# Kernel optimization log

Hardware: AMD Instinct MI355X
Metric: run time of the kernel (lower is better)

## Reference

```python
import jax, jax.numpy as jnp
import numpy as np

B, S, D = 8, 4096, 1024
EPS = 1e-8  # torch F.cosine_similarity default eps


def setup_inputs() -> dict:
    key = jax.random.key(0)
    kx, kwq, kbq, kwk, kbk = jax.random.split(key, 5)
    bound = 1.0 / np.sqrt(D)  # torch nn.Linear default init
    return {
        "x": jax.random.normal(kx, (B, S, D), dtype=jnp.float32),
        "Wq": jax.random.uniform(kwq, (D, D), jnp.float32, -bound, bound),
        "bq": jax.random.uniform(kbq, (D,), jnp.float32, -bound, bound),
        "Wk": jax.random.uniform(kwk, (D, D), jnp.float32, -bound, bound),
        "bk": jax.random.uniform(kbk, (D,), jnp.float32, -bound, bound),
    }


def reference(x, Wq, bq, Wk, bk):
    # ---- RoutingModule ----
    q = jnp.einsum("bsd,ed->bse", x, Wq) + bq                      # [B,S,D]
    x_roll = jnp.roll(x, shift=1, axis=1)                           # roll along seq
    k = jnp.einsum("bsd,ed->bse", x_roll, Wk) + bk                  # [B,S,D]
    qn = q / jnp.maximum(jnp.linalg.norm(q, axis=-1, keepdims=True), EPS)
    kn = k / jnp.maximum(jnp.linalg.norm(k, axis=-1, keepdims=True), EPS)
    cosine_sim = jnp.sum(qn * kn, axis=-1)                          # [B,S]
    p = 0.5 * (1.0 - cosine_sim)
    p = p.at[:, 0].set(1.0)
    b = (p >= 0.5).astype(x.dtype)                                  # [B,S]

    # ---- ragged compaction into padded buffer ----
    # Stable argsort moves selected positions to the front, preserving order.
    order = jnp.argsort(1.0 - b, axis=1)                            # [B,S] int
    gathered = jnp.take_along_axis(x, order[:, :, None], axis=1)    # [B,S,D]
    counts = jnp.sum(b, axis=1).astype(jnp.int32)                   # [B]
    valid = jnp.arange(S)[None, :] < counts[:, None]                # [B,S]
    # Padded to S (static max possible length) for jit-compatibility; torch
    # trims to the batch max, but all rows beyond each count are zeros here too.
    selected_padded = jnp.where(valid[:, :, None], gathered, 0.0)   # [B,S,D]
    return selected_padded, p, b
```

## Files before the change

### kernel.cpp

```cpp
#include <hip/hip_runtime.h>
#include <stdint.h>

#define Bb 8
#define Ss 4096
#define Dd 1024
#define Mm (Bb*Ss)
#define Nn (2*Dd)
#define Kk Dd

typedef _Float16 half8 __attribute__((ext_vector_type(8)));
typedef _Float16 half4v __attribute__((ext_vector_type(4)));
typedef float f32x4 __attribute__((ext_vector_type(4)));

#define LO_SCALE 2048.0f
#define INV_LO_SCALE (1.0f/2048.0f)

__device__ __forceinline__ void gld_lds16(const void* g, void* l) {
  __builtin_amdgcn_global_load_lds(
      (const __attribute__((address_space(1))) unsigned int*)g,
      (__attribute__((address_space(3))) unsigned int*)l, 16, 0, 0);
}

__global__ void split_kernel(const float* __restrict__ src,
                             _Float16* __restrict__ hi,
                             _Float16* __restrict__ lo, int n4) {
  int i = blockIdx.x * 256 + threadIdx.x;
  if (i >= n4) return;
  float4 v = ((const float4*)src)[i];
  _Float16 h0 = (_Float16)v.x, h1 = (_Float16)v.y, h2 = (_Float16)v.z, h3 = (_Float16)v.w;
  _Float16 l0 = (_Float16)((v.x - (float)h0) * LO_SCALE);
  _Float16 l1 = (_Float16)((v.y - (float)h1) * LO_SCALE);
  _Float16 l2 = (_Float16)((v.z - (float)h2) * LO_SCALE);
  _Float16 l3 = (_Float16)((v.w - (float)h3) * LO_SCALE);
  ((half4v*)hi)[i] = (half4v){h0, h1, h2, h3};
  ((half4v*)lo)[i] = (half4v){l0, l1, l2, l3};
}

__global__ __launch_bounds__(256, 2)
void gemm_split(const _Float16* __restrict__ AhG, const _Float16* __restrict__ AlG,
                const _Float16* __restrict__ BhG, const _Float16* __restrict__ BlG,
                const float* __restrict__ bq, const float* __restrict__ bk,
                float* __restrict__ C) {
  __shared__ __align__(16) _Float16 AsH[128 * 32];
  __shared__ __align__(16) _Float16 AsL[128 * 32];
  __shared__ __align__(16) _Float16 BsH[128 * 32];
  __shared__ __align__(16) _Float16 BsL[128 * 32];

  const int tid  = threadIdx.x;
  const int wave = tid >> 6;
  const int lane = tid & 63;
  const int m0 = blockIdx.y * 128;
  const int n0 = blockIdx.x * 128;
  const int wm = (wave >> 1) * 64;
  const int wn = (wave & 1) * 64;

  f32x4 accH[4][4];
  f32x4 accX[4][4];
#pragma unroll
  for (int i = 0; i < 4; ++i)
#pragma unroll
    for (int j = 0; j < 4; ++j) {
      accH[i][j] = (f32x4){0.f, 0.f, 0.f, 0.f};
      accX[i][j] = (f32x4){0.f, 0.f, 0.f, 0.f};
    }

  const int srow = (lane >> 2);
  const int scol = (lane & 3) * 8;

  for (int kt = 0; kt < Kk / 32; ++kt) {
    const int k0 = kt * 32;
#pragma unroll
    for (int it = 0; it < 2; ++it) {
      const int r = wave * 32 + it * 16 + srow;
      const int ldsbase = (wave * 32 + it * 16) * 32;
      const size_t ga = (size_t)(m0 + r) * Kk + k0 + scol;
      const size_t gb = (size_t)(n0 + r) * Kk + k0 + scol;
      gld_lds16(AhG + ga, &AsH[ldsbase]);
      gld_lds16(AlG + ga, &AsL[ldsbase]);
      gld_lds16(BhG + gb, &BsH[ldsbase]);
      gld_lds16(BlG + gb, &BsL[ldsbase]);
    }
    __syncthreads();

    const int fr = (lane & 15);
    const int fk = (lane >> 4) * 8;
    half8 bh[4], bl[4];
#pragma unroll
    for (int j = 0; j < 4; ++j) {
      bh[j] = *(const half8*)&BsH[(wn + 16 * j + fr) * 32 + fk];
      bl[j] = *(const half8*)&BsL[(wn + 16 * j + fr) * 32 + fk];
    }
#pragma unroll
    for (int i = 0; i < 4; ++i) {
      half8 ah = *(const half8*)&AsH[(wm + 16 * i + fr) * 32 + fk];
      half8 al = *(const half8*)&AsL[(wm + 16 * i + fr) * 32 + fk];
#pragma unroll
      for (int j = 0; j < 4; ++j) {
        accH[i][j] = __builtin_amdgcn_mfma_f32_16x16x32_f16(ah, bh[j], accH[i][j], 0, 0, 0);
        accX[i][j] = __builtin_amdgcn_mfma_f32_16x16x32_f16(ah, bl[j], accX[i][j], 0, 0, 0);
        accX[i][j] = __builtin_amdgcn_mfma_f32_16x16x32_f16(al, bh[j], accX[i][j], 0, 0, 0);
      }
    }
    __syncthreads();
  }

  const int quad = (lane >> 4);
#pragma unroll
  for (int j = 0; j < 4; ++j) {
    const int n = n0 + wn + 16 * j + (lane & 15);
    const float bias = (n < Dd) ? bq[n] : bk[n - Dd];
#pragma unroll
    for (int i = 0; i < 4; ++i) {
      const int row0 = m0 + wm + 16 * i + quad * 4;
#pragma unroll
      for (int r = 0; r < 4; ++r) {
        float v = accH[i][j][r] + accX[i][j][r] * INV_LO_SCALE + bias;
        C[(size_t)(row0 + r) * Nn + n] = v;
      }
    }
  }
}

__global__ void cos_pass(const float* __restrict__ QK,
                         float* __restrict__ p_out, float* __restrict__ b_out) {
  const int s = blockIdx.x * 4 + (threadIdx.x >> 6);
  const int lane = threadIdx.x & 63;
  if (s >= Mm) return;
  if ((s & (Ss - 1)) == 0) {
    if (lane == 0) { p_out[s] = 1.0f; b_out[s] = 1.0f; }
    return;
  }
  const float* qrow = QK + (size_t)s * Nn;
  const float* krow = QK + (size_t)(s - 1) * Nn + Dd;
  float dot = 0.f, nq = 0.f, nk = 0.f;
#pragma unroll
  for (int e = lane * 4; e < Dd; e += 256) {
    float4 qv = *(const float4*)&qrow[e];
    float4 kv = *(const float4*)&krow[e];
    dot += qv.x * kv.x + qv.y * kv.y + qv.z * kv.z + qv.w * kv.w;
    nq  += qv.x * qv.x + qv.y * qv.y + qv.z * qv.z + qv.w * qv.w;
    nk  += kv.x * kv.x + kv.y * kv.y + kv.z * kv.z + kv.w * kv.w;
  }
#pragma unroll
  for (int off = 32; off > 0; off >>= 1) {
    dot += __shfl_xor(dot, off);
    nq  += __shfl_xor(nq,  off);
    nk  += __shfl_xor(nk,  off);
  }
  if (lane == 0) {
    float denom = fmaxf(sqrtf(nq), 1e-8f) * fmaxf(sqrtf(nk), 1e-8f);
    float cs = dot / denom;
    float p = 0.5f * (1.0f - cs);
    p_out[s] = p;
    b_out[s] = (p >= 0.5f) ? 1.0f : 0.0f;
  }
}

__global__ void scan_flags(const float* __restrict__ b_out,
                           int* __restrict__ sel, int* __restrict__ counts) {
  const int b = blockIdx.x;
  const int tid = threadIdx.x;
  const int lane = tid & 63;
  const int w = tid >> 6;
  __shared__ int wtot[4];
  int running = 0;
  for (int c = 0; c < Ss / 256; ++c) {
    const int i = c * 256 + tid;
    const bool f = b_out[b * Ss + i] != 0.0f;
    unsigned long long m = __ballot(f);
    int pre = __popcll(m & ((1ull << lane) - 1ull));
    if (lane == 0) wtot[w] = __popcll(m);
    __syncthreads();
    int woff = 0;
#pragma unroll
    for (int ww = 0; ww < 4; ++ww)
      if (ww < w) woff += wtot[ww];
    int tot = wtot[0] + wtot[1] + wtot[2] + wtot[3];
    if (f) sel[b * Ss + running + woff + pre] = i;
    running += tot;
    __syncthreads();
  }
  if (tid == 0) counts[b] = running;
}

__global__ void write_out(const float* __restrict__ x, const int* __restrict__ sel,
                          const int* __restrict__ counts, float* __restrict__ out) {
  const int blk = blockIdx.x;
  const int b = blk >> 12;
  const int r = blk & (Ss - 1);
  const int tid = threadIdx.x;
  float4 v = {0.f, 0.f, 0.f, 0.f};
  if (r < counts[b]) {
    const int src = sel[b * Ss + r];
    v = *(const float4*)&x[((size_t)b * Ss + src) * Dd + tid * 4];
  }
  *(float4*)&out[(size_t)blk * Dd + tid * 4] = v;
}

extern "C" void kernel_launch(void* const* d_in, const int* in_sizes, int n_in,
                              void* d_out, int out_size, void* d_ws, size_t ws_size,
                              hipStream_t stream) {
  const float* x  = (const float*)d_in[0];
  const float* Wq = (const float*)d_in[1];
  const float* bq = (const float*)d_in[2];
  const float* Wk = (const float*)d_in[3];
  const float* bk = (const float*)d_in[4];
  float* out = (float*)d_out;

  uint8_t* w = (uint8_t*)d_ws;
  _Float16* XH = (_Float16*)w;             w += (size_t)Mm * Kk * 2;
  _Float16* XL = (_Float16*)w;             w += (size_t)Mm * Kk * 2;
  _Float16* WH = (_Float16*)w;             w += (size_t)Nn * Kk * 2;
  _Float16* WL = (_Float16*)w;             w += (size_t)Nn * Kk * 2;
  float*    QK = (float*)w;                w += (size_t)Mm * Nn * 4;
  int*      sel = (int*)w;                 w += (size_t)Mm * 4;
  int*      counts = (int*)w;              w += 64;

  float* p_out = out + (size_t)Mm * Dd;
  float* b_out = p_out + Mm;

  {
    int n4 = Mm * Kk / 4;
    split_kernel<<<n4 / 256, 256, 0, stream>>>(x, XH, XL, n4);
    int w4 = Dd * Dd / 4;
    split_kernel<<<w4 / 256, 256, 0, stream>>>(Wq, WH, WL, w4);
    split_kernel<<<w4 / 256, 256, 0, stream>>>(Wk, WH + (size_t)Dd * Dd, WL + (size_t)Dd * Dd, w4);
  }
  {
    dim3 grid(Nn / 128, Mm / 128);
    gemm_split<<<grid, 256, 0, stream>>>(XH, XL, WH, WL, bq, bk, QK);
  }
  cos_pass<<<Mm / 4, 256, 0, stream>>>(QK, p_out, b_out);
  scan_flags<<<Bb, 256, 0, stream>>>(b_out, sel, counts);
  write_out<<<Mm, 256, 0, stream>>>(x, sel, counts, out);
}
```

Measured before the change: 776.7 us.

## Reformulate cosine via precomputed Wq^T Wk Gram matrix and norm-only GEMM

```diff
diff --git a/kernel.cpp b/kernel.cpp
--- a/kernel.cpp
+++ b/kernel.cpp
@@ -5,8 +5,7 @@
 #define Ss 4096
 #define Dd 1024
 #define Mm (Bb*Ss)
-#define Nn (2*Dd)
-#define Kk Dd
+#define Kk 1024
 
 typedef _Float16 half8 __attribute__((ext_vector_type(8)));
 typedef _Float16 half4v __attribute__((ext_vector_type(4)));
@@ -36,26 +35,119 @@
   ((half4v*)lo)[i] = (half4v){l0, l1, l2, l3};
 }
 
-__global__ __launch_bounds__(256, 2)
-void gemm_split(const _Float16* __restrict__ AhG, const _Float16* __restrict__ AlG,
-                const _Float16* __restrict__ BhG, const _Float16* __restrict__ BlG,
-                const float* __restrict__ bq, const float* __restrict__ bk,
-                float* __restrict__ C) {
+__global__ void split_x(const float* __restrict__ X, const float* __restrict__ u,
+                        const float* __restrict__ v,
+                        _Float16* __restrict__ Xh, _Float16* __restrict__ Xl,
+                        float* __restrict__ a_u, float* __restrict__ a_v) {
+  const int s = blockIdx.x * 4 + (threadIdx.x >> 6);
+  const int lane = threadIdx.x & 63;
+  float au = 0.f, av = 0.f;
+#pragma unroll
+  for (int c = 0; c < 4; ++c) {
+    const int e = c * 256 + lane * 4;
+    float4 xv = *(const float4*)&X[(size_t)s * Dd + e];
+    float4 uv = *(const float4*)&u[e];
+    float4 vv = *(const float4*)&v[e];
+    _Float16 h0 = (_Float16)xv.x, h1 = (_Float16)xv.y, h2 = (_Float16)xv.z, h3 = (_Float16)xv.w;
+    _Float16 l0 = (_Float16)((xv.x - (float)h0) * LO_SCALE);
+    _Float16 l1 = (_Float16)((xv.y - (float)h1) * LO_SCALE);
+    _Float16 l2 = (_Float16)((xv.z - (float)h2) * LO_SCALE);
+    _Float16 l3 = (_Float16)((xv.w - (float)h3) * LO_SCALE);
+    *(half4v*)&Xh[(size_t)s * Dd + e] = (half4v){h0, h1, h2, h3};
+    *(half4v*)&Xl[(size_t)s * Dd + e] = (half4v){l0, l1, l2, l3};
+    au += uv.x * xv.x + uv.y * xv.y + uv.z * xv.z + uv.w * xv.w;
+    av += vv.x * xv.x + vv.y * xv.y + vv.z * xv.z + vv.w * xv.w;
+  }
+#pragma unroll
+  for (int off = 32; off > 0; off >>= 1) {
+    au += __shfl_xor(au, off);
+    av += __shfl_xor(av, off);
+  }
+  if (lane == 0) { a_u[s] = au; a_v[s] = av; }
+}
+
+__global__ __launch_bounds__(256)
+void gemm_g(const float* __restrict__ Wq, const float* __restrict__ Wk,
+            float* __restrict__ G) {
+  __shared__ float As[16][64];
+  __shared__ float Bs[16][64];
+  const int t = threadIdx.x;
+  const int m0 = blockIdx.y * 64, n0 = blockIdx.x * 64;
+  float acc[4][4];
+#pragma unroll
+  for (int a = 0; a < 4; ++a)
+#pragma unroll
+    for (int b = 0; b < 4; ++b) acc[a][b] = 0.f;
+  for (int kc = 0; kc < 64; ++kc) {
+    const int k0 = kc * 16;
+#pragma unroll
+    for (int l = 0; l < 4; ++l) {
+      const int idx = l * 256 + t;
+      const int kk = idx >> 6, mm = idx & 63;
+      As[kk][mm] = Wq[(size_t)(k0 + kk) * Dd + m0 + mm];
+      Bs[kk][mm] = Wk[(size_t)(k0 + kk) * Dd + n0 + mm];
+    }
+    __syncthreads();
+    const int tm = (t & 15) * 4, tn = (t >> 4) * 4;
+#pragma unroll
+    for (int k = 0; k < 16; ++k) {
+      float4 a4 = *(const float4*)&As[k][tm];
+      float4 b4 = *(const float4*)&Bs[k][tn];
+      const float aa[4] = {a4.x, a4.y, a4.z, a4.w};
+      const float bb[4] = {b4.x, b4.y, b4.z, b4.w};
+#pragma unroll
+      for (int a = 0; a < 4; ++a)
+#pragma unroll
+        for (int b = 0; b < 4; ++b) acc[a][b] += aa[a] * bb[b];
+    }
+    __syncthreads();
+  }
+  const int tm = (t & 15) * 4, tn = (t >> 4) * 4;
+#pragma unroll
+  for (int a = 0; a < 4; ++a)
+#pragma unroll
+    for (int b = 0; b < 4; ++b)
+      G[(size_t)(m0 + tm + a) * Dd + n0 + tn + b] = acc[a][b];
+}
+
+__global__ void uv_pass(const float* __restrict__ Wq, const float* __restrict__ Wk,
+                        const float* __restrict__ bq, const float* __restrict__ bk,
+                        float* __restrict__ u, float* __restrict__ v) {
+  const int d = blockIdx.x * 256 + threadIdx.x;
+  const int which = blockIdx.y;
+  const float* W = which ? Wq : Wk;
+  const float* bb = which ? bk : bq;
+  float acc = 0.f;
+#pragma unroll 4
+  for (int e = 0; e < Dd; ++e) acc += bb[e] * W[(size_t)e * Dd + d];
+  if (which) v[d] = acc; else u[d] = acc;
+}
+
+__global__ void c_pass(const float* __restrict__ bq, const float* __restrict__ bk,
+                       float* __restrict__ c) {
+  const int lane = threadIdx.x;
+  float a = 0.f;
+#pragma unroll
+  for (int i = 0; i < 16; ++i) a += bq[lane * 16 + i] * bk[lane * 16 + i];
+#pragma unroll
+  for (int off = 32; off > 0; off >>= 1) a += __shfl_xor(a, off);
+  if (lane == 0) *c = a;
+}
+
+__global__ __launch_bounds__(256, 4)
+void gemm_y(const _Float16* __restrict__ Ah, const _Float16* __restrict__ Al,
+            const _Float16* __restrict__ Bh, const _Float16* __restrict__ Bl,
+            float* __restrict__ Y) {
   __shared__ __align__(16) _Float16 AsH[128 * 32];
   __shared__ __align__(16) _Float16 AsL[128 * 32];
   __shared__ __align__(16) _Float16 BsH[128 * 32];
   __shared__ __align__(16) _Float16 BsL[128 * 32];
-
-  const int tid  = threadIdx.x;
-  const int wave = tid >> 6;
-  const int lane = tid & 63;
-  const int m0 = blockIdx.y * 128;
-  const int n0 = blockIdx.x * 128;
-  const int wm = (wave >> 1) * 64;
-  const int wn = (wave & 1) * 64;
-
-  f32x4 accH[4][4];
-  f32x4 accX[4][4];
+  const int tid = threadIdx.x;
+  const int wave = tid >> 6, lane = tid & 63;
+  const int m0 = blockIdx.y * 128, n0 = blockIdx.x * 128;
+  const int wm = (wave >> 1) * 64, wn = (wave & 1) * 64;
+
+  f32x4 accH[4][4], accX[4][4];
 #pragma unroll
   for (int i = 0; i < 4; ++i)
 #pragma unroll
@@ -63,37 +155,38 @@
       accH[i][j] = (f32x4){0.f, 0.f, 0.f, 0.f};
       accX[i][j] = (f32x4){0.f, 0.f, 0.f, 0.f};
     }
-
-  const int srow = (lane >> 2);
-  const int scol = (lane & 3) * 8;
+  const int srow = lane >> 2, c8 = lane & 3;
 
   for (int kt = 0; kt < Kk / 32; ++kt) {
     const int k0 = kt * 32;
 #pragma unroll
     for (int it = 0; it < 2; ++it) {
-      const int r = wave * 32 + it * 16 + srow;
-      const int ldsbase = (wave * 32 + it * 16) * 32;
-      const size_t ga = (size_t)(m0 + r) * Kk + k0 + scol;
-      const size_t gb = (size_t)(n0 + r) * Kk + k0 + scol;
-      gld_lds16(AhG + ga, &AsH[ldsbase]);
-      gld_lds16(AlG + ga, &AsL[ldsbase]);
-      gld_lds16(BhG + gb, &BsH[ldsbase]);
-      gld_lds16(BlG + gb, &BsL[ldsbase]);
-    }
-    __syncthreads();
-
-    const int fr = (lane & 15);
-    const int fk = (lane >> 4) * 8;
+      const int R = wave * 32 + it * 16 + srow;
+      const int sg = c8 ^ ((R >> 2) & 3);
+      const int ldsoff = (wave * 32 + it * 16) * 32;
+      const size_t ga = (size_t)(m0 + R) * Kk + k0 + sg * 8;
+      const size_t gb = (size_t)(n0 + R) * Kk + k0 + sg * 8;
+      gld_lds16(Ah + ga, &AsH[ldsoff]);
+      gld_lds16(Al + ga, &AsL[ldsoff]);
+      gld_lds16(Bh + gb, &BsH[ldsoff]);
+      gld_lds16(Bl + gb, &BsL[ldsoff]);
+    }
+    __syncthreads();
+    const int fr = lane & 15, g = lane >> 4;
     half8 bh[4], bl[4];
 #pragma unroll
     for (int j = 0; j < 4; ++j) {
-      bh[j] = *(const half8*)&BsH[(wn + 16 * j + fr) * 32 + fk];
-      bl[j] = *(const half8*)&BsL[(wn + 16 * j + fr) * 32 + fk];
+      const int R = wn + 16 * j + fr;
+      const int slot = g ^ ((R >> 2) & 3);
+      bh[j] = *(const half8*)&BsH[R * 32 + slot * 8];
+      bl[j] = *(const half8*)&BsL[R * 32 + slot * 8];
     }
 #pragma unroll
     for (int i = 0; i < 4; ++i) {
-      half8 ah = *(const half8*)&AsH[(wm + 16 * i + fr) * 32 + fk];
-      half8 al = *(const half8*)&AsL[(wm + 16 * i + fr) * 32 + fk];
+      const int R = wm + 16 * i + fr;
+      const int slot = g ^ ((R >> 2) & 3);
+      half8 ah = *(const half8*)&AsH[R * 32 + slot * 8];
+      half8 al = *(const half8*)&AsL[R * 32 + slot * 8];
 #pragma unroll
       for (int j = 0; j < 4; ++j) {
         accH[i][j] = __builtin_amdgcn_mfma_f32_16x16x32_f16(ah, bh[j], accH[i][j], 0, 0, 0);
@@ -103,52 +196,130 @@
     }
     __syncthreads();
   }
-
-  const int quad = (lane >> 4);
+  const int quad = lane >> 4;
 #pragma unroll
   for (int j = 0; j < 4; ++j) {
     const int n = n0 + wn + 16 * j + (lane & 15);
-    const float bias = (n < Dd) ? bq[n] : bk[n - Dd];
 #pragma unroll
     for (int i = 0; i < 4; ++i) {
       const int row0 = m0 + wm + 16 * i + quad * 4;
 #pragma unroll
-      for (int r = 0; r < 4; ++r) {
-        float v = accH[i][j][r] + accX[i][j][r] * INV_LO_SCALE + bias;
-        C[(size_t)(row0 + r) * Nn + n] = v;
+      for (int r = 0; r < 4; ++r)
+        Y[(size_t)(row0 + r) * Dd + n] = accH[i][j][r] + accX[i][j][r] * INV_LO_SCALE;
+    }
+  }
+}
+
+__global__ __launch_bounds__(256, 4)
+void gemm_norm(const _Float16* __restrict__ Ah, const _Float16* __restrict__ Bh,
+               const float* __restrict__ bq, const float* __restrict__ bk,
+               float* __restrict__ partials) {
+  __shared__ __align__(16) _Float16 AsH[128 * 32];
+  __shared__ __align__(16) _Float16 BsH[128 * 32];
+  const int tid = threadIdx.x;
+  const int wave = tid >> 6, lane = tid & 63;
+  const int m0 = blockIdx.y * 128, n0 = blockIdx.x * 128;
+  const int wm = (wave >> 1) * 64, wn = (wave & 1) * 64;
+
+  f32x4 acc[4][4];
+#pragma unroll
+  for (int i = 0; i < 4; ++i)
+#pragma unroll
+    for (int j = 0; j < 4; ++j) acc[i][j] = (f32x4){0.f, 0.f, 0.f, 0.f};
+
+  const int srow = lane >> 2, c8 = lane & 3;
+  for (int kt = 0; kt < Kk / 32; ++kt) {
+    const int k0 = kt * 32;
+#pragma unroll
+    for (int it = 0; it < 2; ++it) {
+      const int R = wave * 32 + it * 16 + srow;
+      const int sg = c8 ^ ((R >> 2) & 3);
+      const int ldsoff = (wave * 32 + it * 16) * 32;
+      gld_lds16(Ah + (size_t)(m0 + R) * Kk + k0 + sg * 8, &AsH[ldsoff]);
+      gld_lds16(Bh + (size_t)(n0 + R) * Kk + k0 + sg * 8, &BsH[ldsoff]);
+    }
+    __syncthreads();
+    const int fr = lane & 15, g = lane >> 4;
+    half8 bh[4];
+#pragma unroll
+    for (int j = 0; j < 4; ++j) {
+      const int R = wn + 16 * j + fr;
+      const int slot = g ^ ((R >> 2) & 3);
+      bh[j] = *(const half8*)&BsH[R * 32 + slot * 8];
+    }
+#pragma unroll
+    for (int i = 0; i < 4; ++i) {
+      const int R = wm + 16 * i + fr;
+      const int slot = g ^ ((R >> 2) & 3);
+      half8 ah = *(const half8*)&AsH[R * 32 + slot * 8];
+#pragma unroll
+      for (int j = 0; j < 4; ++j)
+        acc[i][j] = __builtin_amdgcn_mfma_f32_16x16x32_f16(ah, bh[j], acc[i][j], 0, 0, 0);
+    }
+    __syncthreads();
+  }
+  const int quad = lane >> 4;
+  float bias_j[4];
+#pragma unroll
+  for (int j = 0; j < 4; ++j) {
+    const int n = n0 + wn + 16 * j + (lane & 15);
+    bias_j[j] = (n < Dd) ? bq[n] : bk[n - Dd];
+  }
+  const int slot = blockIdx.x * 2 + (wave & 1);
+#pragma unroll
+  for (int i = 0; i < 4; ++i) {
+#pragma unroll
+    for (int r = 0; r < 4; ++r) {
+      float vsum = 0.f;
+#pragma unroll
+      for (int j = 0; j < 4; ++j) {
+        float q = acc[i][j][r] + bias_j[j];
+        vsum += q * q;
       }
-    }
-  }
-}
-
-__global__ void cos_pass(const float* __restrict__ QK,
+      vsum += __shfl_xor(vsum, 1);
+      vsum += __shfl_xor(vsum, 2);
+      vsum += __shfl_xor(vsum, 4);
+      vsum += __shfl_xor(vsum, 8);
+      if ((lane & 15) == 0)
+        partials[(size_t)slot * Mm + (m0 + wm + 16 * i + quad * 4 + r)] = vsum;
+    }
+  }
+}
+
+__global__ void cos_pass(const float* __restrict__ X, const float* __restrict__ Y,
+                         const float* __restrict__ P, const float* __restrict__ a_u,
+                         const float* __restrict__ a_v, const float* __restrict__ cptr,
                          float* __restrict__ p_out, float* __restrict__ b_out) {
   const int s = blockIdx.x * 4 + (threadIdx.x >> 6);
   const int lane = threadIdx.x & 63;
-  if (s >= Mm) return;
   if ((s & (Ss - 1)) == 0) {
     if (lane == 0) { p_out[s] = 1.0f; b_out[s] = 1.0f; }
     return;
   }
-  const float* qrow = QK + (size_t)s * Nn;
-  const float* krow = QK + (size_t)(s - 1) * Nn + Dd;
-  float dot = 0.f, nq = 0.f, nk = 0.f;
-#pragma unroll
-  for (int e = lane * 4; e < Dd; e += 256) {
-    float4 qv = *(const float4*)&qrow[e];
-    float4 kv = *(const float4*)&krow[e];
-    dot += qv.x * kv.x + qv.y * kv.y + qv.z * kv.z + qv.w * kv.w;
-    nq  += qv.x * qv.x + qv.y * qv.y + qv.z * qv.z + qv.w * qv.w;
-    nk  += kv.x * kv.x + kv.y * kv.y + kv.z * kv.z + kv.w * kv.w;
-  }
-#pragma unroll
-  for (int off = 32; off > 0; off >>= 1) {
-    dot += __shfl_xor(dot, off);
-    nq  += __shfl_xor(nq,  off);
-    nk  += __shfl_xor(nk,  off);
-  }
+  const float* xs = X + (size_t)s * Dd;
+  const float* ym = Y + (size_t)(s - 1) * Dd;
+  float d = 0.f;
+#pragma unroll
+  for (int c = 0; c < 4; ++c) {
+    const int e = c * 256 + lane * 4;
+    float4 xv = *(const float4*)&xs[e];
+    float4 yv = *(const float4*)&ym[e];
+    d += xv.x * yv.x + xv.y * yv.y + xv.z * yv.z + xv.w * yv.w;
+  }
+#pragma unroll
+  for (int off = 32; off > 0; off >>= 1) d += __shfl_xor(d, off);
+
+  float pn = 0.f;
+  if (lane < 32) pn = P[(size_t)lane * Mm + ((lane < 16) ? s : (s - 1))];
+  pn += __shfl_xor(pn, 1);
+  pn += __shfl_xor(pn, 2);
+  pn += __shfl_xor(pn, 4);
+  pn += __shfl_xor(pn, 8);
+  float nk2 = __shfl(pn, 16);
   if (lane == 0) {
-    float denom = fmaxf(sqrtf(nq), 1e-8f) * fmaxf(sqrtf(nk), 1e-8f);
+    float nq2 = pn;
+    float dot = d + a_u[s - 1] + a_v[s] + *cptr;
+    float denom = fmaxf(sqrtf(nq2), 1e-8f) * fmaxf(sqrtf(nk2), 1e-8f);
     float cs = dot / denom;
     float p = 0.5f * (1.0f - cs);
     p_out[s] = p;
@@ -208,29 +379,36 @@
   float* out = (float*)d_out;
 
   uint8_t* w = (uint8_t*)d_ws;
-  _Float16* XH = (_Float16*)w;             w += (size_t)Mm * Kk * 2;
-  _Float16* XL = (_Float16*)w;             w += (size_t)Mm * Kk * 2;
-  _Float16* WH = (_Float16*)w;             w += (size_t)Nn * Kk * 2;
-  _Float16* WL = (_Float16*)w;             w += (size_t)Nn * Kk * 2;
-  float*    QK = (float*)w;                w += (size_t)Mm * Nn * 4;
-  int*      sel = (int*)w;                 w += (size_t)Mm * 4;
-  int*      counts = (int*)w;              w += 64;
+  _Float16* Xh = (_Float16*)w;   w += (size_t)Mm * Kk * 2;
+  _Float16* Xl = (_Float16*)w;   w += (size_t)Mm * Kk * 2;
+  float*    Y  = (float*)w;      w += (size_t)Mm * Dd * 4;
+  float*    G  = (float*)w;      w += (size_t)Dd * Dd * 4;
+  _Float16* Gh = (_Float16*)w;   w += (size_t)Dd * Dd * 2;
+  _Float16* Gl = (_Float16*)w;   w += (size_t)Dd * Dd * 2;
+  _Float16* Wh = (_Float16*)w;   w += (size_t)2 * Dd * Dd * 2;
+  _Float16* Wl = (_Float16*)w;   w += (size_t)2 * Dd * Dd * 2;
+  float* partials = (float*)w;   w += (size_t)32 * Mm * 4;
+  float* a_u = (float*)w;        w += (size_t)Mm * 4;
+  float* a_v = (float*)w;        w += (size_t)Mm * 4;
+  float* u   = (float*)w;        w += Dd * 4;
+  float* v   = (float*)w;        w += Dd * 4;
+  float* cpt = (float*)w;        w += 64;
+  int*   sel = (int*)w;          w += (size_t)Mm * 4;
+  int*   counts = (int*)w;       w += 64;
 
   float* p_out = out + (size_t)Mm * Dd;
   float* b_out = p_out + Mm;
 
-  {
-    int n4 = Mm * Kk / 4;
-    split_kernel<<<n4 / 256, 256, 0, stream>>>(x, XH, XL, n4);
-    int w4 = Dd * Dd / 4;
-    split_kernel<<<w4 / 256, 256, 0, stream>>>(Wq, WH, WL, w4);
-    split_kernel<<<w4 / 256, 256, 0, stream>>>(Wk, WH + (size_t)Dd * Dd, WL + (size_t)Dd * Dd, w4);
-  }
-  {
-    dim3 grid(Nn / 128, Mm / 128);
-    gemm_split<<<grid, 256, 0, stream>>>(XH, XL, WH, WL, bq, bk, QK);
-  }
-  cos_pass<<<Mm / 4, 256, 0, stream>>>(QK, p_out, b_out);
+  gemm_g<<<dim3(16, 16), 256, 0, stream>>>(Wq, Wk, G);
+  uv_pass<<<dim3(4, 2), 256, 0, stream>>>(Wq, Wk, bq, bk, u, v);
+  c_pass<<<1, 64, 0, stream>>>(bq, bk, cpt);
+  split_x<<<Mm / 4, 256, 0, stream>>>(x, u, v, Xh, Xl, a_u, a_v);
+  split_kernel<<<(Dd * Dd / 4) / 256, 256, 0, stream>>>(G, Gh, Gl, Dd * Dd / 4);
+  split_kernel<<<(Dd * Dd / 4) / 256, 256, 0, stream>>>(Wq, Wh, Wl, Dd * Dd / 4);
+  split_kernel<<<(Dd * Dd / 4) / 256, 256, 0, stream>>>(Wk, Wh + (size_t)Dd * Dd, Wl + (size_t)Dd * Dd, Dd * Dd / 4);
+  gemm_y<<<dim3(Dd / 128, Mm / 128), 256, 0, stream>>>(Xh, Xl, Gh, Gl, Y);
+  gemm_norm<<<dim3(2 * Dd / 128, Mm / 128), 256, 0, stream>>>(Xh, Wh, bq, bk, partials);
+  cos_pass<<<Mm / 4, 256, 0, stream>>>(x, Y, partials, a_u, a_v, cpt, p_out, b_out);
   scan_flags<<<Bb, 256, 0, stream>>>(b_out, sel, counts);
   write_out<<<Mm, 256, 0, stream>>>(x, sel, counts, out);
 }
```

Result: slower. 2.058 ms (+165.0%).
